# Kernel optimization log

Measured on AMD Instinct MI355X. Metric: run time of the kernel, lower is better.

## Reference

```python
import jax, jax.numpy as jnp
import numpy as np

SIZE = (128, 128, 128)  # volume dims (X, Y, Z)
B, N, C = 2, 2097152, 1


def setup_inputs() -> dict:
    key = jax.random.key(0)
    k1, k2 = jax.random.split(key)
    image = jax.random.normal(k1, (B, SIZE[0], SIZE[1], SIZE[2], C), dtype=jnp.float32)
    grid = jax.random.uniform(k2, (B, N, 3), dtype=jnp.float32)  # normalized coords in [0,1]
    return {"image": image, "grid": grid}


def reference(image, grid):
    # image: [B, X, Y, Z, C]; grid: [B, N, 3] normalized -> trilinear sample -> [B, N, C]
    factor = jnp.array(SIZE, dtype=jnp.float32)
    idx = jnp.clip(grid * factor, 0.001, float(min(SIZE)) - 1.001)  # [B, N, 3]
    x, y, z = idx[..., 0], idx[..., 1], idx[..., 2]
    x1, x2 = jnp.floor(x), jnp.ceil(x)
    y1, y2 = jnp.floor(y), jnp.ceil(y)
    z1, z2 = jnp.floor(z), jnp.ceil(z)

    b = jnp.arange(image.shape[0])[:, None]  # [B, 1] batch index for gathers

    def g(xi, yi, zi):  # corner gather -> [B, N, C]
        return image[b, xi.astype(jnp.int32), yi.astype(jnp.int32), zi.astype(jnp.int32)]

    wx, wx2 = (x - x1)[..., None], (x2 - x)[..., None]
    wy, wy2 = (y - y1)[..., None], (y2 - y)[..., None]
    wz, wz2 = (z - z1)[..., None], (z2 - z)[..., None]

    lerp_y1 = (g(x2, y1, z1) * wx + g(x1, y1, z1) * wx2) * wy2 \
            + (g(x2, y2, z1) * wx + g(x1, y2, z1) * wx2) * wy
    lerp_y2 = (g(x2, y1, z2) * wx + g(x1, y1, z2) * wx2) * wy2 \
            + (g(x2, y2, z2) * wx + g(x1, y2, z2) * wx2) * wy
    return lerp_y2 * wz + lerp_y1 * wz2
```

## Files before the change

kernel.cpp:

```cpp
#include <hip/hip_runtime.h>
#include <hip/hip_fp16.h>


#define TOTAL   (2 * 2097152)
#define LOG2N   21
#define VOL     (128 * 128 * 128)
#define NVOX    (2 * VOL)

__global__ __launch_bounds__(256)
void ImageWarped_cvt_fp16_kernel(const float* __restrict__ in,
                                 __half* __restrict__ out)
{
    const int i = blockIdx.x * 256 + threadIdx.x;
    const float4 v = ((const float4*)in)[i];
    union { __half2 h2[2]; uint2 u; } p;
    p.h2[0] = __floats2half2_rn(v.x, v.y);
    p.h2[1] = __floats2half2_rn(v.z, v.w);
    ((uint2*)out)[i] = p.u;
}

__global__ __launch_bounds__(256)
void ImageWarped_trilinear_h2_kernel(const __half* __restrict__ image,
                                     const float* __restrict__ grid,
                                     float* __restrict__ out)
{
    const int batch = blockIdx.x & 1;
    const int s     = (blockIdx.x >> 1) * 256 + threadIdx.x;
    const int i     = (batch << LOG2N) | s;

    const float gx = grid[3 * i + 0];
    const float gy = grid[3 * i + 1];
    const float gz = grid[3 * i + 2];

    const __half* __restrict__ img = image + ((size_t)batch << LOG2N);

    const float xf = fminf(fmaxf(gx * 128.0f, 0.001f), 126.999f);
    const float yf = fminf(fmaxf(gy * 128.0f, 0.001f), 126.999f);
    const float zf = fminf(fmaxf(gz * 128.0f, 0.001f), 126.999f);

    const float x1f = floorf(xf), x2f = ceilf(xf);
    const float y1f = floorf(yf), y2f = ceilf(yf);
    const float z1f = floorf(zf), z2f = ceilf(zf);

    const float wx  = xf - x1f, wx2 = x2f - xf;
    const float wy  = yf - y1f, wy2 = y2f - yf;
    const float wz  = zf - z1f, wz2 = z2f - zf;

    const int ix1 = (int)x1f, ix2 = (int)x2f;
    const int iy1 = (int)y1f, iy2 = (int)y2f;
    const int iz1 = (int)z1f;

    const int bx1 = ix1 << 14, bx2 = ix2 << 14;
    const int by1 = iy1 << 7,  by2 = iy2 << 7;

    const int ze = min(iz1 & ~1, 124);
    const int sh = (iz1 - ze) << 4;

    const float  ww  = wz2, wwz = wz;
    auto zfetch = [&](int off) -> float {
        const uint2 u = *(const uint2*)(img + off + ze);
        unsigned long long w = ((unsigned long long)u.y << 32) | u.x;
        w >>= sh;
        union { unsigned int u32; __half2 h; } c;
        c.u32 = (unsigned int)w;
        const float2 f = __half22float2(c.h);
        return f.x * ww + f.y * wwz;
    };

    const float q11 = zfetch(bx1 + by1);
    const float q21 = zfetch(bx2 + by1);
    const float q12 = zfetch(bx1 + by2);
    const float q22 = zfetch(bx2 + by2);

    out[i] = (q21 * wx + q11 * wx2) * wy2
           + (q22 * wx + q12 * wx2) * wy;
}

__global__ __launch_bounds__(256)
void ImageWarped_trilinear_f_kernel(const float* __restrict__ image,
                                    const float* __restrict__ grid,
                                    float* __restrict__ out)
{
    const int i = blockIdx.x * 256 + threadIdx.x;
    if (i >= TOTAL) return;

    const float gx = grid[3 * i + 0];
    const float gy = grid[3 * i + 1];
    const float gz = grid[3 * i + 2];

    const int b = i >> LOG2N;
    const float* __restrict__ img = image + (size_t)b * VOL;

    const float xf = fminf(fmaxf(gx * 128.0f, 0.001f), 126.999f);
    const float yf = fminf(fmaxf(gy * 128.0f, 0.001f), 126.999f);
    const float zf = fminf(fmaxf(gz * 128.0f, 0.001f), 126.999f);

    const float x1f = floorf(xf), x2f = ceilf(xf);
    const float y1f = floorf(yf), y2f = ceilf(yf);
    const float z1f = floorf(zf), z2f = ceilf(zf);

    const float wx  = xf - x1f, wx2 = x2f - xf;
    const float wy  = yf - y1f, wy2 = y2f - yf;
    const float wz  = zf - z1f, wz2 = z2f - zf;

    const int ix1 = (int)x1f, ix2 = (int)x2f;
    const int iy1 = (int)y1f, iy2 = (int)y2f;
    const int iz1 = (int)z1f, iz2 = (int)z2f;

    const int bx1 = ix1 << 14, bx2 = ix2 << 14;
    const int by1 = iy1 << 7,  by2 = iy2 << 7;

    const float c111 = img[bx1 + by1 + iz1];
    const float c211 = img[bx2 + by1 + iz1];
    const float c121 = img[bx1 + by2 + iz1];
    const float c221 = img[bx2 + by2 + iz1];
    const float c112 = img[bx1 + by1 + iz2];
    const float c212 = img[bx2 + by1 + iz2];
    const float c122 = img[bx1 + by2 + iz2];
    const float c222 = img[bx2 + by2 + iz2];

    const float lerp_y1 = (c211 * wx + c111 * wx2) * wy2
                        + (c221 * wx + c121 * wx2) * wy;
    const float lerp_y2 = (c212 * wx + c112 * wx2) * wy2
                        + (c222 * wx + c122 * wx2) * wy;

    out[i] = lerp_y2 * wz + lerp_y1 * wz2;
}

extern "C" void kernel_launch(void* const* d_in, const int* in_sizes, int n_in,
                              void* d_out, int out_size, void* d_ws, size_t ws_size,
                              hipStream_t stream)
{
    const float* image = (const float*)d_in[0];
    const float* grid  = (const float*)d_in[1];
    float* out = (float*)d_out;

    const int blocks = (TOTAL + 255) / 256;

    if (ws_size >= (size_t)NVOX * sizeof(__half)) {
        __half* img16 = (__half*)d_ws;
        ImageWarped_cvt_fp16_kernel<<<NVOX / 4 / 256, 256, 0, stream>>>(image, img16);
        ImageWarped_trilinear_h2_kernel<<<blocks, 256, 0, stream>>>(img16, grid, out);
    } else {
        ImageWarped_trilinear_f_kernel<<<blocks, 256, 0, stream>>>(image, grid, out);
    }
}
```

Before: 174.7 us.

## Pack all eight fp16 trilinear corners into one 16-byte record per voxel

```diff
diff --git a/kernel.cpp b/kernel.cpp
--- a/kernel.cpp
+++ b/kernel.cpp
@@ -6,6 +6,81 @@
 #define LOG2N   21
 #define VOL     (128 * 128 * 128)
 #define NVOX    (2 * VOL)
+
+__global__ __launch_bounds__(256)
+void ImageWarped_build_rec_kernel(const float* __restrict__ in,
+                                  uint4* __restrict__ rec)
+{
+    const int idx = blockIdx.x * 256 + threadIdx.x;
+    const int v   = idx & (VOL - 1);
+    const int x   = v >> 14;
+    const int y   = (v >> 7) & 127;
+    const int z   = v & 127;
+    const int zp  = min(z + 1, 127);
+    const int xo  = (x < 127) ? (1 << 14) : 0;
+    const int yo  = (y < 127) ? (1 << 7)  : 0;
+
+    const float* __restrict__ r11 = in + (idx - z);
+    const float* __restrict__ r21 = r11 + xo;
+    const float* __restrict__ r12 = r11 + yo;
+    const float* __restrict__ r22 = r21 + yo;
+
+    union { __half2 h; unsigned u; } p0, p1, p2, p3;
+    p0.h = __floats2half2_rn(r11[z], r11[zp]);
+    p1.h = __floats2half2_rn(r21[z], r21[zp]);
+    p2.h = __floats2half2_rn(r12[z], r12[zp]);
+    p3.h = __floats2half2_rn(r22[z], r22[zp]);
+
+    rec[idx] = make_uint4(p0.u, p1.u, p2.u, p3.u);
+}
+
+__global__ __launch_bounds__(256)
+void ImageWarped_trilinear_rec_kernel(const uint4* __restrict__ rec,
+                                      const float* __restrict__ grid,
+                                      float* __restrict__ out)
+{
+    const int batch = blockIdx.x & 1;
+    const int s     = (blockIdx.x >> 1) * 256 + threadIdx.x;
+    const int i     = (batch << LOG2N) | s;
+
+    const float gx = __builtin_nontemporal_load(grid + 3 * i + 0);
+    const float gy = __builtin_nontemporal_load(grid + 3 * i + 1);
+    const float gz = __builtin_nontemporal_load(grid + 3 * i + 2);
+
+    const float xf = fminf(fmaxf(gx * 128.0f, 0.001f), 126.999f);
+    const float yf = fminf(fmaxf(gy * 128.0f, 0.001f), 126.999f);
+    const float zf = fminf(fmaxf(gz * 128.0f, 0.001f), 126.999f);
+
+    const float x1f = floorf(xf), x2f = ceilf(xf);
+    const float y1f = floorf(yf), y2f = ceilf(yf);
+    const float z1f = floorf(zf), z2f = ceilf(zf);
+
+    const float wx  = xf - x1f, wx2 = x2f - xf;
+    const float wy  = yf - y1f, wy2 = y2f - yf;
+    const float wz  = zf - z1f, wz2 = z2f - zf;
+
+    const int ix1 = (int)x1f;
+    const int iy1 = (int)y1f;
+    const int iz1 = (int)z1f;
+
+    const int base = (batch << LOG2N) + (ix1 << 14) + (iy1 << 7) + iz1;
+    const uint4 u = rec[base];
+
+    auto zlerp = [&](unsigned w) -> float {
+        union { unsigned u32; __half2 h; } c;
+        c.u32 = w;
+        const float2 f = __half22float2(c.h);
+        return f.x * wz2 + f.y * wz;
+    };
+    const float q11 = zlerp(u.x);
+    const float q21 = zlerp(u.y);
+    const float q12 = zlerp(u.z);
+    const float q22 = zlerp(u.w);
+
+    const float r = (q21 * wx + q11 * wx2) * wy2
+                  + (q22 * wx + q12 * wx2) * wy;
+    __builtin_nontemporal_store(r, out + i);
+}
 
 __global__ __launch_bounds__(256)
 void ImageWarped_cvt_fp16_kernel(const float* __restrict__ in,
@@ -137,7 +212,11 @@
 
     const int blocks = (TOTAL + 255) / 256;
 
-    if (ws_size >= (size_t)NVOX * sizeof(__half)) {
+    if (ws_size >= (size_t)NVOX * sizeof(uint4)) {
+        uint4* rec = (uint4*)d_ws;
+        ImageWarped_build_rec_kernel<<<NVOX / 256, 256, 0, stream>>>(image, rec);
+        ImageWarped_trilinear_rec_kernel<<<blocks, 256, 0, stream>>>(rec, grid, out);
+    } else if (ws_size >= (size_t)NVOX * sizeof(__half)) {
         __half* img16 = (__half*)d_ws;
         ImageWarped_cvt_fp16_kernel<<<NVOX / 4 / 256, 256, 0, stream>>>(image, img16);
         ImageWarped_trilinear_h2_kernel<<<blocks, 256, 0, stream>>>(img16, grid, out);
```

Result: no change. 177.3 us (+1.4%).

## Prebuild per-voxel 8-corner fp16 records so each sample needs one 16-byte gather

Applied to the files above, without the earlier changes.

```diff
diff --git a/kernel.cpp b/kernel.cpp
--- a/kernel.cpp
+++ b/kernel.cpp
@@ -6,6 +6,112 @@
 #define LOG2N   21
 #define VOL     (128 * 128 * 128)
 #define NVOX    (2 * VOL)
+
+typedef __attribute__((ext_vector_type(4))) float fx4;
+
+__global__ __launch_bounds__(256)
+void ImageWarped_build_rec4_kernel(const float* __restrict__ in,
+                                   uint4* __restrict__ rec)
+{
+    const int t    = blockIdx.x * 256 + threadIdx.x;
+    const int idx0 = t << 2;
+    const int v    = idx0 & (VOL - 1);
+    const int x    = v >> 14;
+    const int y    = (v >> 7) & 127;
+    const int z0   = v & 127;
+    const int xo   = (x < 127) ? (1 << 14) : 0;
+    const int yo   = (y < 127) ? (1 << 7)  : 0;
+
+    const float* __restrict__ r11 = in + (idx0 - z0);
+    const float* __restrict__ r21 = r11 + xo;
+    const float* __restrict__ r12 = r11 + yo;
+    const float* __restrict__ r22 = r21 + yo;
+
+    const int zn = min(z0 + 4, 127);
+    const float4 a11 = *(const float4*)(r11 + z0); const float e11 = r11[zn];
+    const float4 a21 = *(const float4*)(r21 + z0); const float e21 = r21[zn];
+    const float4 a12 = *(const float4*)(r12 + z0); const float e12 = r12[zn];
+    const float4 a22 = *(const float4*)(r22 + z0); const float e22 = r22[zn];
+
+    union { __half2 h; unsigned u; } p;
+    #define PAIR(lo, hi) (p.h = __floats2half2_rn((lo), (hi)), p.u)
+    rec[idx0 + 0] = make_uint4(PAIR(a11.x, a11.y), PAIR(a21.x, a21.y),
+                               PAIR(a12.x, a12.y), PAIR(a22.x, a22.y));
+    rec[idx0 + 1] = make_uint4(PAIR(a11.y, a11.z), PAIR(a21.y, a21.z),
+                               PAIR(a12.y, a12.z), PAIR(a22.y, a22.z));
+    rec[idx0 + 2] = make_uint4(PAIR(a11.z, a11.w), PAIR(a21.z, a21.w),
+                               PAIR(a12.z, a12.w), PAIR(a22.z, a22.w));
+    rec[idx0 + 3] = make_uint4(PAIR(a11.w, e11),   PAIR(a21.w, e21),
+                               PAIR(a12.w, e12),   PAIR(a22.w, e22));
+    #undef PAIR
+}
+
+struct SampleW { int base; float wx, wx2, wy, wy2, wz, wz2; };
+
+__device__ __forceinline__ SampleW mk_sample(float gx, float gy, float gz)
+{
+    SampleW s;
+    const float xf = fminf(fmaxf(gx * 128.0f, 0.001f), 126.999f);
+    const float yf = fminf(fmaxf(gy * 128.0f, 0.001f), 126.999f);
+    const float zf = fminf(fmaxf(gz * 128.0f, 0.001f), 126.999f);
+    const float x1f = floorf(xf), x2f = ceilf(xf);
+    const float y1f = floorf(yf), y2f = ceilf(yf);
+    const float z1f = floorf(zf), z2f = ceilf(zf);
+    s.wx = xf - x1f; s.wx2 = x2f - xf;
+    s.wy = yf - y1f; s.wy2 = y2f - yf;
+    s.wz = zf - z1f; s.wz2 = z2f - zf;
+    s.base = ((int)x1f << 14) + ((int)y1f << 7) + (int)z1f;
+    return s;
+}
+
+__device__ __forceinline__ float fold_sample(const uint4 u, const SampleW& s)
+{
+    union { unsigned u32; __half2 h; } c;
+    c.u32 = u.x; const float2 f11 = __half22float2(c.h);
+    c.u32 = u.y; const float2 f21 = __half22float2(c.h);
+    c.u32 = u.z; const float2 f12 = __half22float2(c.h);
+    c.u32 = u.w; const float2 f22 = __half22float2(c.h);
+    const float q11 = f11.x * s.wz2 + f11.y * s.wz;
+    const float q21 = f21.x * s.wz2 + f21.y * s.wz;
+    const float q12 = f12.x * s.wz2 + f12.y * s.wz;
+    const float q22 = f22.x * s.wz2 + f22.y * s.wz;
+    return (q21 * s.wx + q11 * s.wx2) * s.wy2
+         + (q22 * s.wx + q12 * s.wx2) * s.wy;
+}
+
+__global__ __launch_bounds__(256)
+void ImageWarped_trilinear_rec4_kernel(const uint4* __restrict__ rec,
+                                       const float* __restrict__ grid,
+                                       float* __restrict__ out)
+{
+    const int batch = blockIdx.x & 1;
+    const int g     = (blockIdx.x >> 1) * 256 + threadIdx.x;
+    const int i0    = (batch << LOG2N) | (g << 2);
+
+    const fx4* gp = (const fx4*)(grid + 3 * (size_t)i0);
+    const fx4 a = __builtin_nontemporal_load(gp + 0);
+    const fx4 b = __builtin_nontemporal_load(gp + 1);
+    const fx4 d = __builtin_nontemporal_load(gp + 2);
+
+    const uint4* __restrict__ rb = rec + ((size_t)batch << LOG2N);
+
+    const SampleW s0 = mk_sample(a.x, a.y, a.z);
+    const SampleW s1 = mk_sample(a.w, b.x, b.y);
+    const SampleW s2 = mk_sample(b.z, b.w, d.x);
+    const SampleW s3 = mk_sample(d.y, d.z, d.w);
+
+    const uint4 u0 = rb[s0.base];
+    const uint4 u1 = rb[s1.base];
+    const uint4 u2 = rb[s2.base];
+    const uint4 u3 = rb[s3.base];
+
+    fx4 r;
+    r.x = fold_sample(u0, s0);
+    r.y = fold_sample(u1, s1);
+    r.z = fold_sample(u2, s2);
+    r.w = fold_sample(u3, s3);
+    __builtin_nontemporal_store(r, (fx4*)(out + i0));
+}
 
 __global__ __launch_bounds__(256)
 void ImageWarped_cvt_fp16_kernel(const float* __restrict__ in,
@@ -135,13 +241,15 @@
     const float* grid  = (const float*)d_in[1];
     float* out = (float*)d_out;
 
-    const int blocks = (TOTAL + 255) / 256;
-
-    if (ws_size >= (size_t)NVOX * sizeof(__half)) {
+    if (ws_size >= (size_t)NVOX * sizeof(uint4)) {
+        uint4* rec = (uint4*)d_ws;
+        ImageWarped_build_rec4_kernel<<<NVOX / 4 / 256, 256, 0, stream>>>(image, rec);
+        ImageWarped_trilinear_rec4_kernel<<<TOTAL / 4 / 256, 256, 0, stream>>>(rec, grid, out);
+    } else if (ws_size >= (size_t)NVOX * sizeof(__half)) {
         __half* img16 = (__half*)d_ws;
         ImageWarped_cvt_fp16_kernel<<<NVOX / 4 / 256, 256, 0, stream>>>(image, img16);
-        ImageWarped_trilinear_h2_kernel<<<blocks, 256, 0, stream>>>(img16, grid, out);
+        ImageWarped_trilinear_h2_kernel<<<(TOTAL + 255) / 256, 256, 0, stream>>>(img16, grid, out);
     } else {
-        ImageWarped_trilinear_f_kernel<<<blocks, 256, 0, stream>>>(image, grid, out);
+        ImageWarped_trilinear_f_kernel<<<(TOTAL + 255) / 256, 256, 0, stream>>>(image, grid, out);
     }
 }
```

New measurement: 187.8 us. 1.07x slower.

## Repack fp16 volume into 2x2 xy-quad interleaved layout for trilinear gathers

Applied to the files above, without the earlier changes.

```diff
diff --git a/kernel.cpp b/kernel.cpp
--- a/kernel.cpp
+++ b/kernel.cpp
@@ -8,21 +8,45 @@
 #define NVOX    (2 * VOL)
 
 __global__ __launch_bounds__(256)
-void ImageWarped_cvt_fp16_kernel(const float* __restrict__ in,
-                                 __half* __restrict__ out)
+void ImageWarped_build_q_kernel(const float* __restrict__ in,
+                                __half* __restrict__ outv)
 {
-    const int i = blockIdx.x * 256 + threadIdx.x;
-    const float4 v = ((const float4*)in)[i];
-    union { __half2 h2[2]; uint2 u; } p;
-    p.h2[0] = __floats2half2_rn(v.x, v.y);
-    p.h2[1] = __floats2half2_rn(v.z, v.w);
-    ((uint2*)out)[i] = p.u;
+    const int t  = blockIdx.x * 256 + threadIdx.x;
+    const int zq = t & 31;
+    const int yh = (t >> 5) & 63;
+    const int xh = (t >> 11) & 63;
+    const int b  = t >> 17;
+    const int z0 = zq << 2;
+
+    const float* __restrict__ r00 = in + b * VOL + ((xh * 2) << 14)
+                                       + ((yh * 2) << 7) + z0;
+    const float* __restrict__ r10 = r00 + (1 << 14);
+    const float* __restrict__ r01 = r00 + (1 << 7);
+    const float* __restrict__ r11 = r10 + (1 << 7);
+
+    const float4 v00 = *(const float4*)r00;
+    const float4 v10 = *(const float4*)r10;
+    const float4 v01 = *(const float4*)r01;
+    const float4 v11 = *(const float4*)r11;
+
+    union { __half2 h; unsigned u; } p;
+    #define H2Q(a, b_) (p.h = __floats2half2_rn((a), (b_)), p.u)
+    const uint4 A = make_uint4(H2Q(v00.x, v10.x), H2Q(v01.x, v11.x),
+                               H2Q(v00.y, v10.y), H2Q(v01.y, v11.y));
+    const uint4 Bq = make_uint4(H2Q(v00.z, v10.z), H2Q(v01.z, v11.z),
+                                H2Q(v00.w, v10.w), H2Q(v01.w, v11.w));
+    #undef H2Q
+
+    const size_t hb = ((size_t)b << 21)
+                    + ((size_t)((((xh << 6) | yh) << 7) | z0) << 2);
+    *(uint4*)(outv + hb)     = A;
+    *(uint4*)(outv + hb + 8) = Bq;
 }
 
 __global__ __launch_bounds__(256)
-void ImageWarped_trilinear_h2_kernel(const __half* __restrict__ image,
-                                     const float* __restrict__ grid,
-                                     float* __restrict__ out)
+void ImageWarped_trilinear_q_kernel(const __half* __restrict__ image,
+                                    const float* __restrict__ grid,
+                                    float* __restrict__ out)
 {
     const int batch = blockIdx.x & 1;
     const int s     = (blockIdx.x >> 1) * 256 + threadIdx.x;
@@ -46,31 +70,38 @@
     const float wy  = yf - y1f, wy2 = y2f - yf;
     const float wz  = zf - z1f, wz2 = z2f - zf;
 
-    const int ix1 = (int)x1f, ix2 = (int)x2f;
-    const int iy1 = (int)y1f, iy2 = (int)y2f;
+    const int ix1 = (int)x1f;
+    const int iy1 = (int)y1f;
     const int iz1 = (int)z1f;
 
-    const int bx1 = ix1 << 14, bx2 = ix2 << 14;
-    const int by1 = iy1 << 7,  by2 = iy2 << 7;
+    const int sx = ix1 & 1, sy = iy1 & 1;
+    const int xh = ix1 >> 1, yh = iy1 >> 1;
 
-    const int ze = min(iz1 & ~1, 124);
-    const int sh = (iz1 - ze) << 4;
+    const int base00 = (((xh << 6) | yh) << 9) + (iz1 << 2);
+    const int base10 = base00 + (sx << 15);
+    const int base01 = base00 + (sy << 9);
+    const int base11 = base10 + (sy << 9);
 
-    const float  ww  = wz2, wwz = wz;
-    auto zfetch = [&](int off) -> float {
-        const uint2 u = *(const uint2*)(img + off + ze);
-        unsigned long long w = ((unsigned long long)u.y << 32) | u.x;
-        w >>= sh;
-        union { unsigned int u32; __half2 h; } c;
-        c.u32 = (unsigned int)w;
+    const uint4 L00 = *(const uint4*)(img + base00);
+    const uint4 L10 = *(const uint4*)(img + base10);
+    const uint4 L01 = *(const uint4*)(img + base01);
+    const uint4 L11 = *(const uint4*)(img + base11);
+
+    const int shA = sx << 4;
+    const int shB = 16 - shA;
+    const float ww = wz2, wwz = wz;
+
+    auto zl = [&](unsigned d0, unsigned d1, int sh) -> float {
+        union { unsigned u32; __half2 h; } c;
+        c.u32 = ((d0 >> sh) & 0xffffu) | (((d1 >> sh) & 0xffffu) << 16);
         const float2 f = __half22float2(c.h);
         return f.x * ww + f.y * wwz;
     };
 
-    const float q11 = zfetch(bx1 + by1);
-    const float q21 = zfetch(bx2 + by1);
-    const float q12 = zfetch(bx1 + by2);
-    const float q22 = zfetch(bx2 + by2);
+    const float q11 = zl(sy ? L00.y : L00.x, sy ? L00.w : L00.z, shA);
+    const float q21 = zl(sy ? L10.y : L10.x, sy ? L10.w : L10.z, shB);
+    const float q12 = zl(sy ? L01.x : L01.y, sy ? L01.z : L01.w, shA);
+    const float q22 = zl(sy ? L11.x : L11.y, sy ? L11.z : L11.w, shB);
 
     out[i] = (q21 * wx + q11 * wx2) * wy2
            + (q22 * wx + q12 * wx2) * wy;
@@ -138,9 +169,9 @@
     const int blocks = (TOTAL + 255) / 256;
 
     if (ws_size >= (size_t)NVOX * sizeof(__half)) {
-        __half* img16 = (__half*)d_ws;
-        ImageWarped_cvt_fp16_kernel<<<NVOX / 4 / 256, 256, 0, stream>>>(image, img16);
-        ImageWarped_trilinear_h2_kernel<<<blocks, 256, 0, stream>>>(img16, grid, out);
+        __half* imgq = (__half*)d_ws;
+        ImageWarped_build_q_kernel<<<NVOX / 16 / 256, 256, 0, stream>>>(image, imgq);
+        ImageWarped_trilinear_q_kernel<<<blocks, 256, 0, stream>>>(imgq, grid, out);
     } else {
         ImageWarped_trilinear_f_kernel<<<blocks, 256, 0, stream>>>(image, grid, out);
     }
```

Measured after the change: 167.6 us. -4.1%, faster.
